# Performance work log

Measured on AMD Instinct MI355X. Metric: run time of the kernel, lower is better.

The kernel has to match this reference:

```python
import jax, jax.numpy as jnp
import numpy as np

N_HEADS = 16


def setup_inputs() -> dict:
    key = jax.random.key(0)
    ks = jax.random.split(key, 5)
    E = 1024
    x = jax.random.normal(ks[0], (2, 2048, E), dtype=jnp.float32)
    s = 1.0 / np.sqrt(E)
    Wq = jax.random.normal(ks[1], (E, E), dtype=jnp.float32) * s
    Wk = jax.random.normal(ks[2], (E, E), dtype=jnp.float32) * s
    Wv = jax.random.normal(ks[3], (E, E), dtype=jnp.float32) * s
    Wo = jax.random.normal(ks[4], (E, E), dtype=jnp.float32) * s
    bo = jnp.zeros((E,), dtype=jnp.float32)
    return {"x": x, "Wq": Wq, "Wk": Wk, "Wv": Wv, "Wo": Wo, "bo": bo}


def reference(x, Wq, Wk, Wv, Wo, bo):
    B, S, E = x.shape
    H = N_HEADS
    D = E // H
    # project and split heads: [B, H, S, D]
    def split_heads(y):
        return y.reshape(B, S, H, D).transpose(0, 2, 1, 3)
    q = split_heads(x @ Wq)
    k = split_heads(x @ Wk)
    v = split_heads(x @ Wv)
    # full score matrix [B, H, S, S]
    scores = jnp.einsum('bhqd,bhkd->bhqk', q, k)
    causal = jnp.triu(jnp.ones((S, S), dtype=bool), k=1)
    scores = jnp.where(causal, -jnp.inf, scores)
    attn = jax.nn.softmax(scores / jnp.sqrt(jnp.float32(D)), axis=-1)
    # dropout rate is 0.0 -> identity
    ctx = jnp.einsum('bhqk,bhkd->bhqd', attn, v)
    ctx = ctx.transpose(0, 2, 1, 3).reshape(B, S, E)
    return ctx @ Wo + bo
```

## Files before the change

kernel.cpp:

```cpp
#include <hip/hip_runtime.h>
#include <stdint.h>


#define N_HEADS 16
#define HD 64
#define SEQ 2048
#define EMB 1024

typedef __attribute__((ext_vector_type(8))) short s16x8;
typedef __attribute__((ext_vector_type(4))) float f32x4;

#define QSCALE 0.18033688f

__device__ __forceinline__ short f2b(float f) {
  union { float f; uint32_t u; } v; v.f = f;
  uint32_t u = v.u;
  u += 0x7fffu + ((u >> 16) & 1u);
  return (short)(u >> 16);
}

__device__ __forceinline__ uint32_t pk2(float a, float b) {
  union { float f; uint32_t u; } x, y; x.f = a; y.f = b;
  return ((x.u + 0x8000u) >> 16) | ((y.u + 0x8000u) & 0xffff0000u);
}

__device__ __forceinline__ float exp2a(float x) {
  float r; asm("v_exp_f32 %0, %1" : "=v"(r) : "v"(x)); return r;
}

__device__ __forceinline__ void gll16(const void* g, void* l) {
  __builtin_amdgcn_global_load_lds((const __attribute__((address_space(1))) void*)g,
                                   (__attribute__((address_space(3))) void*)l, 16, 0, 0);
}

#define SWZ(row, chunk) ((((row) * 8) + ((chunk) ^ ((row) & 7))) * 8)

__global__ __launch_bounds__(256) void k_prep(const float* __restrict__ x,
                                              const float* __restrict__ W0,
                                              const float* __restrict__ W1,
                                              const float* __restrict__ W2,
                                              const float* __restrict__ W3,
                                              short* __restrict__ xb,
                                              short* __restrict__ wt) {
  const int z = blockIdx.x, t = threadIdx.x;
  if (z < 4096) {
    int i = z * 256 + t;
    float4 v = ((const float4*)x)[i];
    short4 o;
    o.x = f2b(v.x); o.y = f2b(v.y); o.z = f2b(v.z); o.w = f2b(v.w);
    ((short4*)xb)[i] = o;
  } else {
    __shared__ float tile[32][33];
    int bz = z - 4096;
    int w = bz >> 10, rem = bz & 1023;
    int bn = (rem & 31) * 32, bk = (rem >> 5) * 32;
    const float* W = w == 0 ? W0 : w == 1 ? W1 : w == 2 ? W2 : W3;
    short* o = wt + (size_t)w * EMB * EMB;
    int tx = t & 31, ty = t >> 5;
    for (int i = ty; i < 32; i += 8)
      tile[i][tx] = W[(size_t)(bk + i) * EMB + bn + tx];
    __syncthreads();
    for (int i = ty; i < 32; i += 8)
      o[(size_t)(bn + i) * EMB + bk + tx] = f2b(tile[tx][i]);
  }
}

template <int MODE, int MT>
__global__ __launch_bounds__(256) void k_gemm(const short* __restrict__ A,
                                              const short* __restrict__ BT,
                                              void* __restrict__ outp,
                                              const float* __restrict__ bias) {
  constexpr int BM = MT * 32;
  constexpr bool SWAP = (MODE != 2);
  constexpr bool DBUF = (MODE == 1);
  constexpr int NB = DBUF ? 2 : 1;
  constexpr int MAIN = NB * (BM * 32 + 128 * 32);
  constexpr int EPIL = (MODE == 1) ? 0 : 128 * 132;
  constexpr int SMSZ = MAIN > EPIL ? MAIN : EPIL;
  __shared__ alignas(16) short smem[SMSZ];

  const int t = threadIdx.x;
  const int m0 = blockIdx.x * BM;
  const int n0 = blockIdx.y * 128;
  const int wave = t >> 6, lane = t & 63;
  const int wm = (wave >> 1) * (MT * 16), wn = (wave & 1) * 64;
  const int ml = lane & 15, quad = lane >> 4;
  const int k0 = quad * 8;
  const int lr = lane >> 2, lc = (lane & 3) * 8;

  auto stage = [&](int kb, int p) {
    short* as = smem + p * (BM * 32);
    short* bs = smem + NB * (BM * 32) + p * (128 * 32);
#pragma unroll
    for (int rr = 0; rr < MT / 2; rr++) {
      int arow = wave * (MT * 8) + rr * 16;
      gll16(A + (size_t)(m0 + arow + lr) * EMB + kb + lc, &as[arow * 32]);
    }
#pragma unroll
    for (int rr = 0; rr < 2; rr++) {
      int brow = wave * 32 + rr * 16;
      gll16(BT + (size_t)(n0 + brow + lr) * EMB + kb + lc, &bs[brow * 32]);
    }
  };

  f32x4 acc[MT][4] = {};
  int pb = 0;

  if (DBUF) stage(0, 0);
  for (int kb = 0; kb < EMB; kb += 32) {
    __syncthreads();
    if (DBUF) {
      if (kb + 32 < EMB) stage(kb + 32, pb ^ 1);
    } else {
      stage(kb, 0);
      __syncthreads();
    }
    const short* as = smem + (DBUF ? pb : 0) * (BM * 32);
    const short* bs = smem + NB * (BM * 32) + (DBUF ? pb : 0) * (128 * 32);
    s16x8 af[MT], bf[4];
#pragma unroll
    for (int i = 0; i < MT; i++) af[i] = *(const s16x8*)&as[(wm + i * 16 + ml) * 32 + k0];
#pragma unroll
    for (int i = 0; i < 4; i++) bf[i] = *(const s16x8*)&bs[(wn + i * 16 + ml) * 32 + k0];
#pragma unroll
    for (int mt = 0; mt < MT; mt++)
#pragma unroll
      for (int nt = 0; nt < 4; nt++)
        acc[mt][nt] = SWAP
          ? __builtin_amdgcn_mfma_f32_16x16x32_bf16(bf[nt], af[mt], acc[mt][nt], 0, 0, 0)
          : __builtin_amdgcn_mfma_f32_16x16x32_bf16(af[mt], bf[nt], acc[mt][nt], 0, 0, 0);
    pb ^= 1;
  }

  if (MODE == 0) {
    __syncthreads();
    short* Vls = smem;
    const int wsel = blockIdx.y >> 3;
    const float qs = (wsel == 0) ? QSCALE : 1.0f;
    const int n0l = (blockIdx.y & 7) * 128;
#pragma unroll
    for (int mt = 0; mt < MT; mt++) {
      int mr = wm + mt * 16 + ml;
#pragma unroll
      for (int nt = 0; nt < 4; nt++) {
        uint2 w;
        w.x = pk2(acc[mt][nt][0] * qs, acc[mt][nt][1] * qs);
        w.y = pk2(acc[mt][nt][2] * qs, acc[mt][nt][3] * qs);
        *(uint2*)&Vls[mr * 132 + wn + nt * 16 + quad * 4] = w;
      }
    }
    __syncthreads();
    short* ob = (short*)outp + (size_t)wsel * (4u * 1024 * 1024);
    const int bb = m0 >> 11, ss0 = m0 & (SEQ - 1);
#pragma unroll
    for (int i = 0; i < 8; i++) {
      int mrow = i * 16 + (t >> 4);
      int ncol = (t & 15) * 8;
      int e = n0l + ncol, hh = e >> 6, dd = e & 63;
      *(uint4*)&ob[(((size_t)(bb * N_HEADS + hh) * SEQ) + ss0 + mrow) * 64 + dd] =
          *(const uint4*)&Vls[mrow * 132 + ncol];
    }
  } else if (MODE == 2) {
    __syncthreads();
    short* Vls = smem;
#pragma unroll
    for (int nt = 0; nt < 4; nt++) {
      int nl = wn + nt * 16 + ml;
#pragma unroll
      for (int mt = 0; mt < MT; mt++) {
        int mc = wm + mt * 16 + quad * 4;
        uint2 w;
        w.x = pk2(acc[mt][nt][0], acc[mt][nt][1]);
        w.y = pk2(acc[mt][nt][2], acc[mt][nt][3]);
        *(uint2*)&Vls[nl * 132 + mc] = w;
      }
    }
    __syncthreads();
    short* obv = (short*)outp + (size_t)8 * 1024 * 1024;
    const int e0 = n0;
    const int bb = m0 >> 11, ss0 = m0 & (SEQ - 1);
#pragma unroll
    for (int i = 0; i < 8; i++) {
      int nl = i * 16 + (t >> 4);
      int mc = (t & 15) * 8;
      int e = e0 + nl, hh = e >> 6, dd = e & 63;
      *(uint4*)&obv[((size_t)((bb * N_HEADS + hh) * HD + dd)) * SEQ + ss0 + mc] =
          *(const uint4*)&Vls[nl * 132 + mc];
    }
  } else {
    float* of = (float*)outp;
    f32x4 bv[4];
#pragma unroll
    for (int nt = 0; nt < 4; nt++)
      bv[nt] = *(const f32x4*)&bias[n0 + wn + nt * 16 + quad * 4];
#pragma unroll
    for (int mt = 0; mt < MT; mt++) {
      int mg = m0 + wm + mt * 16 + ml;
#pragma unroll
      for (int nt = 0; nt < 4; nt++) {
        f32x4 w = acc[mt][nt] + bv[nt];
        *(f32x4*)&of[(size_t)mg * EMB + n0 + wn + nt * 16 + quad * 4] = w;
      }
    }
  }
}

__global__ __launch_bounds__(256) void k_attn(const short* __restrict__ Q,
                                              const short* __restrict__ K,
                                              const short* __restrict__ Vt,
                                              short* __restrict__ ctx) {
  __shared__ alignas(16) short UQP[64 * 72];
  __shared__ alignas(16) short Ks0[64 * 64], Ks1[64 * 64];
  __shared__ alignas(16) short Vs0[64 * 64], Vs1[64 * 64];

  const int t = threadIdx.x, wave = t >> 6, lane = t & 63;
  const int ml = lane & 15, quad = lane >> 4;
  const int bh = blockIdx.x;
  const int qb = 31 - (int)blockIdx.y;
  const size_t base = (size_t)bh * SEQ * HD;
  const int q0 = qb * 64, wq = q0 + wave * 16;

  const int sr = lane >> 3;
  const int sc = ((lane & 7) ^ sr) * 8;

#pragma unroll
  for (int i = 0; i < 2; i++) {
    int r8 = wave * 16 + i * 8;
    gll16(Q + base + (size_t)(q0 + r8 + sr) * HD + sc, &UQP[r8 * 64]);
  }
  auto stageKV = [&](int kt, short* kd, short* vd) {
    const int kbase = kt * 64;
#pragma unroll
    for (int i = 0; i < 2; i++) {
      int r8 = wave * 16 + i * 8;
      gll16(K + base + (size_t)(kbase + r8 + sr) * HD + sc, &kd[r8 * 64]);
      gll16(Vt + base + (size_t)(r8 + sr) * SEQ + kbase + sc, &vd[r8 * 64]);
    }
  };

  f32x4 cacc[4] = {};
  float li = 0.f;
  short* Pw = &UQP[wave * 16 * 72];

  stageKV(0, Ks0, Vs0);
  __syncthreads();

  s16x8 qf[2];
#pragma unroll
  for (int c = 0; c < 2; c++)
    qf[c] = *(const s16x8*)&UQP[SWZ(wave * 16 + ml, 4 * c + quad)];
  __syncthreads();

  auto tile_body = [&](int kt, const short* kd, const short* vd) {
    const int kbase = kt * 64;
    if (kbase > wq + 15) return;
    const bool diag = (kbase + 63 > wq);
    f32x4 st[4];
#pragma unroll
    for (int nt = 0; nt < 4; nt++) {
      int row = nt * 16 + ml;
      s16x8 kf0 = *(const s16x8*)&kd[SWZ(row, quad)];
      s16x8 kf1 = *(const s16x8*)&kd[SWZ(row, 4 + quad)];
      f32x4 z = {};
      z = __builtin_amdgcn_mfma_f32_16x16x32_bf16(kf0, qf[0], z, 0, 0, 0);
      st[nt] = __builtin_amdgcn_mfma_f32_16x16x32_bf16(kf1, qf[1], z, 0, 0, 0);
    }
    const int qg = wq + ml;
    float rsum = 0.f;
#pragma unroll
    for (int nt = 0; nt < 4; nt++) {
      float p0 = exp2a(st[nt][0]);
      float p1 = exp2a(st[nt][1]);
      float p2 = exp2a(st[nt][2]);
      float p3 = exp2a(st[nt][3]);
      if (diag) {
        int kk = kbase + nt * 16 + quad * 4;
        if (kk + 0 > qg) p0 = 0.f;
        if (kk + 1 > qg) p1 = 0.f;
        if (kk + 2 > qg) p2 = 0.f;
        if (kk + 3 > qg) p3 = 0.f;
      }
      rsum += (p0 + p1) + (p2 + p3);
      uint2 w; w.x = pk2(p0, p1); w.y = pk2(p2, p3);
      *(uint2*)&Pw[ml * 72 + nt * 16 + quad * 4] = w;
    }
    li += rsum;
    __builtin_amdgcn_wave_barrier();

    s16x8 pf[2];
#pragma unroll
    for (int c = 0; c < 2; c++)
      pf[c] = *(const s16x8*)&Pw[ml * 72 + c * 32 + quad * 8];
#pragma unroll
    for (int mt = 0; mt < 4; mt++) {
      int row = mt * 16 + ml;
      s16x8 vf0 = *(const s16x8*)&vd[SWZ(row, quad)];
      s16x8 vf1 = *(const s16x8*)&vd[SWZ(row, 4 + quad)];
      cacc[mt] = __builtin_amdgcn_mfma_f32_16x16x32_bf16(vf0, pf[0], cacc[mt], 0, 0, 0);
      cacc[mt] = __builtin_amdgcn_mfma_f32_16x16x32_bf16(vf1, pf[1], cacc[mt], 0, 0, 0);
    }
  };

  for (int kt = 0; kt <= qb; kt += 2) {
    if (kt + 1 <= qb) stageKV(kt + 1, Ks1, Vs1);
    tile_body(kt, Ks0, Vs0);
    __syncthreads();
    if (kt + 2 <= qb) stageKV(kt + 2, Ks0, Vs0);
    if (kt + 1 <= qb) tile_body(kt + 1, Ks1, Vs1);
    __syncthreads();
  }

  li += __shfl_xor(li, 16, 64);
  li += __shfl_xor(li, 32, 64);
  float inv = 1.0f / li;
#pragma unroll
  for (int mt = 0; mt < 4; mt++) {
    uint2 w;
    w.x = pk2(cacc[mt][0] * inv, cacc[mt][1] * inv);
    w.y = pk2(cacc[mt][2] * inv, cacc[mt][3] * inv);
    *(uint2*)&Pw[ml * 72 + mt * 16 + quad * 4] = w;
  }
  __builtin_amdgcn_wave_barrier();
  const int b = bh >> 4, h = bh & 15;
#pragma unroll
  for (int i = 0; i < 2; i++) {
    int row = i * 8 + (lane >> 3);
    int q = wq + row;
    size_t gbase = ((size_t)(b * SEQ + q)) * EMB + h * 64 + (lane & 7) * 8;
    *(uint4*)&ctx[gbase] = *(const uint4*)&Pw[row * 72 + (lane & 7) * 8];
  }
}

extern "C" void kernel_launch(void* const* d_in, const int* in_sizes, int n_in,
                              void* d_out, int out_size, void* d_ws, size_t ws_size,
                              hipStream_t stream) {
  const float* x  = (const float*)d_in[0];
  const float* Wq = (const float*)d_in[1];
  const float* Wk = (const float*)d_in[2];
  const float* Wv = (const float*)d_in[3];
  const float* Wo = (const float*)d_in[4];
  const float* bo = (const float*)d_in[5];
  float* out = (float*)d_out;

  short* ws = (short*)d_ws;
  short* xb  = ws;
  short* wt  = ws + (size_t)4 * 1024 * 1024;
  short* qkv = ws + (size_t)8 * 1024 * 1024;

  k_prep<<<8192, 256, 0, stream>>>(x, Wq, Wk, Wv, Wo, xb, wt);
  k_gemm<0, 4><<<dim3(32, 16), 256, 0, stream>>>(xb, wt, qkv, nullptr);
  k_gemm<2, 4><<<dim3(32, 8), 256, 0, stream>>>(xb, wt + (size_t)2 * 1024 * 1024, qkv, nullptr);
  k_attn<<<dim3(32, 32), 256, 0, stream>>>(qkv, qkv + (size_t)4 * 1024 * 1024,
                                           qkv + (size_t)8 * 1024 * 1024, xb);
  k_gemm<1, 2><<<dim3(64, 8), 256, 0, stream>>>(xb, wt + (size_t)3 * 1024 * 1024, out, bo);
}
```

Baseline: 186.8 us.

## Switch GEMMs to 32x32x16 MFMA with swizzled LDS and double buffering

Rewrites the projection GEMM kernel to use 32x32x16 bf16 MFMA tiles (2x2 per wave) instead of 16x16x32, adds an XOR swizzle on the LDS layout to avoid bank conflicts, and enables double-buffered staging for all modes. The output projection tile grows from 64x128 to 128x128, halving its grid. This aims to cut LDS reads and conflicts per MFMA and overlap global loads with compute, but the larger tile for the output GEMM gives fewer blocks (256) on a large-CU GPU.

Result: faster. 179.6 us (-3.9%).

```diff
diff --git a/kernel.cpp b/kernel.cpp
--- a/kernel.cpp
+++ b/kernel.cpp
@@ -9,6 +9,7 @@
 
 typedef __attribute__((ext_vector_type(8))) short s16x8;
 typedef __attribute__((ext_vector_type(4))) float f32x4;
+typedef __attribute__((ext_vector_type(16))) float f32x16;
 
 #define QSCALE 0.18033688f
 
@@ -65,70 +66,68 @@
   }
 }
 
-template <int MODE, int MT>
+template <int MODE>
 __global__ __launch_bounds__(256) void k_gemm(const short* __restrict__ A,
                                               const short* __restrict__ BT,
                                               void* __restrict__ outp,
                                               const float* __restrict__ bias) {
-  constexpr int BM = MT * 32;
   constexpr bool SWAP = (MODE != 2);
-  constexpr bool DBUF = (MODE == 1);
-  constexpr int NB = DBUF ? 2 : 1;
-  constexpr int MAIN = NB * (BM * 32 + 128 * 32);
+  constexpr int MAIN = 4 * 4096;
   constexpr int EPIL = (MODE == 1) ? 0 : 128 * 132;
   constexpr int SMSZ = MAIN > EPIL ? MAIN : EPIL;
   __shared__ alignas(16) short smem[SMSZ];
 
   const int t = threadIdx.x;
-  const int m0 = blockIdx.x * BM;
+  const int m0 = blockIdx.x * 128;
   const int n0 = blockIdx.y * 128;
   const int wave = t >> 6, lane = t & 63;
-  const int wm = (wave >> 1) * (MT * 16), wn = (wave & 1) * 64;
-  const int ml = lane & 15, quad = lane >> 4;
-  const int k0 = quad * 8;
-  const int lr = lane >> 2, lc = (lane & 3) * 8;
+  const int wm = (wave >> 1) * 64, wn = (wave & 1) * 64;
+  const int l31 = lane & 31, lh = lane >> 5;
+
+  const int srow = lane >> 2;
+  const int soff = ((lane & 3) ^ (srow & 3)) * 8;
 
   auto stage = [&](int kb, int p) {
-    short* as = smem + p * (BM * 32);
-    short* bs = smem + NB * (BM * 32) + p * (128 * 32);
-#pragma unroll
-    for (int rr = 0; rr < MT / 2; rr++) {
-      int arow = wave * (MT * 8) + rr * 16;
-      gll16(A + (size_t)(m0 + arow + lr) * EMB + kb + lc, &as[arow * 32]);
-    }
-#pragma unroll
-    for (int rr = 0; rr < 2; rr++) {
-      int brow = wave * 32 + rr * 16;
-      gll16(BT + (size_t)(n0 + brow + lr) * EMB + kb + lc, &bs[brow * 32]);
+    short* as = smem + p * 4096;
+    short* bs = smem + 8192 + p * 4096;
+#pragma unroll
+    for (int i = 0; i < 2; i++) {
+      int rb = wave * 32 + i * 16;
+      gll16(A + (size_t)(m0 + rb + srow) * EMB + kb + soff, &as[rb * 32]);
+      gll16(BT + (size_t)(n0 + rb + srow) * EMB + kb + soff, &bs[rb * 32]);
     }
   };
-
-  f32x4 acc[MT][4] = {};
+  auto frd = [&](const short* sb, int row, int kh) -> s16x8 {
+    int c = kh * 2 + lh;
+    return *(const s16x8*)&sb[row * 32 + ((c ^ (row & 3)) * 8)];
+  };
+
+  f32x16 acc[2][2] = {};
   int pb = 0;
-
-  if (DBUF) stage(0, 0);
+  stage(0, 0);
   for (int kb = 0; kb < EMB; kb += 32) {
     __syncthreads();
-    if (DBUF) {
-      if (kb + 32 < EMB) stage(kb + 32, pb ^ 1);
-    } else {
-      stage(kb, 0);
-      __syncthreads();
-    }
-    const short* as = smem + (DBUF ? pb : 0) * (BM * 32);
-    const short* bs = smem + NB * (BM * 32) + (DBUF ? pb : 0) * (128 * 32);
-    s16x8 af[MT], bf[4];
-#pragma unroll
-    for (int i = 0; i < MT; i++) af[i] = *(const s16x8*)&as[(wm + i * 16 + ml) * 32 + k0];
-#pragma unroll
-    for (int i = 0; i < 4; i++) bf[i] = *(const s16x8*)&bs[(wn + i * 16 + ml) * 32 + k0];
-#pragma unroll
-    for (int mt = 0; mt < MT; mt++)
-#pragma unroll
-      for (int nt = 0; nt < 4; nt++)
-        acc[mt][nt] = SWAP
-          ? __builtin_amdgcn_mfma_f32_16x16x32_bf16(bf[nt], af[mt], acc[mt][nt], 0, 0, 0)
-          : __builtin_amdgcn_mfma_f32_16x16x32_bf16(af[mt], bf[nt], acc[mt][nt], 0, 0, 0);
+    if (kb + 32 < EMB) stage(kb + 32, pb ^ 1);
+    const short* as = smem + pb * 4096;
+    const short* bs = smem + 8192 + pb * 4096;
+    s16x8 af[2][2], bf[2][2];
+#pragma unroll
+    for (int mt = 0; mt < 2; mt++)
+#pragma unroll
+      for (int kh = 0; kh < 2; kh++) af[mt][kh] = frd(as, wm + mt * 32 + l31, kh);
+#pragma unroll
+    for (int nt = 0; nt < 2; nt++)
+#pragma unroll
+      for (int kh = 0; kh < 2; kh++) bf[nt][kh] = frd(bs, wn + nt * 32 + l31, kh);
+#pragma unroll
+    for (int mt = 0; mt < 2; mt++)
+#pragma unroll
+      for (int nt = 0; nt < 2; nt++)
+#pragma unroll
+        for (int kh = 0; kh < 2; kh++)
+          acc[mt][nt] = SWAP
+            ? __builtin_amdgcn_mfma_f32_32x32x16_bf16(bf[nt][kh], af[mt][kh], acc[mt][nt], 0, 0, 0)
+            : __builtin_amdgcn_mfma_f32_32x32x16_bf16(af[mt][kh], bf[nt][kh], acc[mt][nt], 0, 0, 0);
     pb ^= 1;
   }
 
@@ -139,15 +138,17 @@
     const float qs = (wsel == 0) ? QSCALE : 1.0f;
     const int n0l = (blockIdx.y & 7) * 128;
 #pragma unroll
-    for (int mt = 0; mt < MT; mt++) {
-      int mr = wm + mt * 16 + ml;
-#pragma unroll
-      for (int nt = 0; nt < 4; nt++) {
-        uint2 w;
-        w.x = pk2(acc[mt][nt][0] * qs, acc[mt][nt][1] * qs);
-        w.y = pk2(acc[mt][nt][2] * qs, acc[mt][nt][3] * qs);
-        *(uint2*)&Vls[mr * 132 + wn + nt * 16 + quad * 4] = w;
-      }
+    for (int mt = 0; mt < 2; mt++) {
+      int mr = wm + mt * 32 + l31;
+#pragma unroll
+      for (int nt = 0; nt < 2; nt++)
+#pragma unroll
+        for (int g = 0; g < 4; g++) {
+          uint2 w;
+          w.x = pk2(acc[mt][nt][4 * g + 0] * qs, acc[mt][nt][4 * g + 1] * qs);
+          w.y = pk2(acc[mt][nt][4 * g + 2] * qs, acc[mt][nt][4 * g + 3] * qs);
+          *(uint2*)&Vls[mr * 132 + wn + nt * 32 + g * 8 + 4 * lh] = w;
+        }
     }
     __syncthreads();
     short* ob = (short*)outp + (size_t)wsel * (4u * 1024 * 1024);
@@ -164,43 +165,47 @@
     __syncthreads();
     short* Vls = smem;
 #pragma unroll
-    for (int nt = 0; nt < 4; nt++) {
-      int nl = wn + nt * 16 + ml;
-#pragma unroll
-      for (int mt = 0; mt < MT; mt++) {
-        int mc = wm + mt * 16 + quad * 4;
-        uint2 w;
-        w.x = pk2(acc[mt][nt][0], acc[mt][nt][1]);
-        w.y = pk2(acc[mt][nt][2], acc[mt][nt][3]);
-        *(uint2*)&Vls[nl * 132 + mc] = w;
-      }
+    for (int nt = 0; nt < 2; nt++) {
+      int nl = wn + nt * 32 + l31;
+#pragma unroll
+      for (int mt = 0; mt < 2; mt++)
+#pragma unroll
+        for (int g = 0; g < 4; g++) {
+          uint2 w;
+          w.x = pk2(acc[mt][nt][4 * g + 0], acc[mt][nt][4 * g + 1]);
+          w.y = pk2(acc[mt][nt][4 * g + 2], acc[mt][nt][4 * g + 3]);
+          *(uint2*)&Vls[nl * 132 + wm + mt * 32 + g * 8 + 4 * lh] = w;
+        }
     }
     __syncthreads();
     short* obv = (short*)outp + (size_t)8 * 1024 * 1024;
-    const int e0 = n0;
     const int bb = m0 >> 11, ss0 = m0 & (SEQ - 1);
 #pragma unroll
     for (int i = 0; i < 8; i++) {
       int nl = i * 16 + (t >> 4);
       int mc = (t & 15) * 8;
-      int e = e0 + nl, hh = e >> 6, dd = e & 63;
+      int e = n0 + nl, hh = e >> 6, dd = e & 63;
       *(uint4*)&obv[((size_t)((bb * N_HEADS + hh) * HD + dd)) * SEQ + ss0 + mc] =
           *(const uint4*)&Vls[nl * 132 + mc];
     }
   } else {
     float* of = (float*)outp;
-    f32x4 bv[4];
-#pragma unroll
-    for (int nt = 0; nt < 4; nt++)
-      bv[nt] = *(const f32x4*)&bias[n0 + wn + nt * 16 + quad * 4];
-#pragma unroll
-    for (int mt = 0; mt < MT; mt++) {
-      int mg = m0 + wm + mt * 16 + ml;
-#pragma unroll
-      for (int nt = 0; nt < 4; nt++) {
-        f32x4 w = acc[mt][nt] + bv[nt];
-        *(f32x4*)&of[(size_t)mg * EMB + n0 + wn + nt * 16 + quad * 4] = w;
-      }
+#pragma unroll
+    for (int mt = 0; mt < 2; mt++) {
+      int mg = m0 + wm + mt * 32 + l31;
+#pragma unroll
+      for (int nt = 0; nt < 2; nt++)
+#pragma unroll
+        for (int g = 0; g < 4; g++) {
+          int ng = n0 + wn + nt * 32 + g * 8 + 4 * lh;
+          f32x4 bv = *(const f32x4*)&bias[ng];
+          f32x4 w;
+          w[0] = acc[mt][nt][4 * g + 0] + bv[0];
+          w[1] = acc[mt][nt][4 * g + 1] + bv[1];
+          w[2] = acc[mt][nt][4 * g + 2] + bv[2];
+          w[3] = acc[mt][nt][4 * g + 3] + bv[3];
+          *(f32x4*)&of[(size_t)mg * EMB + ng] = w;
+        }
     }
   }
 }
@@ -348,9 +353,9 @@
   short* qkv = ws + (size_t)8 * 1024 * 1024;
 
   k_prep<<<8192, 256, 0, stream>>>(x, Wq, Wk, Wv, Wo, xb, wt);
-  k_gemm<0, 4><<<dim3(32, 16), 256, 0, stream>>>(xb, wt, qkv, nullptr);
-  k_gemm<2, 4><<<dim3(32, 8), 256, 0, stream>>>(xb, wt + (size_t)2 * 1024 * 1024, qkv, nullptr);
+  k_gemm<0><<<dim3(32, 16), 256, 0, stream>>>(xb, wt, qkv, nullptr);
+  k_gemm<2><<<dim3(32, 8), 256, 0, stream>>>(xb, wt + (size_t)2 * 1024 * 1024, qkv, nullptr);
   k_attn<<<dim3(32, 32), 256, 0, stream>>>(qkv, qkv + (size_t)4 * 1024 * 1024,
                                            qkv + (size_t)8 * 1024 * 1024, xb);
-  k_gemm<1, 2><<<dim3(64, 8), 256, 0, stream>>>(xb, wt + (size_t)3 * 1024 * 1024, out, bo);
-}
+  k_gemm<1><<<dim3(32, 8), 256, 0, stream>>>(xb, wt + (size_t)3 * 1024 * 1024, out, bo);
+}
```
